# Performance work log

Hardware: AMD Instinct MI355X
Metric: run time of the kernel (lower is better)

The kernel has to match this reference:

```python
import jax, jax.numpy as jnp
import numpy as np

NUM_CORRESPONDENCES = 256
M, N, D = 8192, 8192, 256


def setup_inputs() -> dict:
    key = jax.random.key(0)
    k1, k2 = jax.random.split(key)
    ref = jax.random.normal(k1, (M, D), dtype=jnp.float32)
    src = jax.random.normal(k2, (N, D), dtype=jnp.float32)
    # pairwise_distance(normalized=True) assumes unit-norm features
    ref = ref / jnp.linalg.norm(ref, axis=-1, keepdims=True)
    src = src / jnp.linalg.norm(src, axis=-1, keepdims=True)
    return {"ref_feats": ref, "src_feats": src}


def reference(ref_feats, src_feats):
    # squared pairwise distance for normalized feats: ||r||^2 + ||s||^2 - 2 r.s = 2 - 2 r.s
    dist = 2.0 - 2.0 * jnp.einsum('md,nd->mn', ref_feats, src_feats)  # [M, N]
    scores = jnp.exp(-dist)
    # dual normalization: row-normalized * col-normalized
    ref_scores = scores / jnp.sum(scores, axis=1, keepdims=True)
    src_scores = scores / jnp.sum(scores, axis=0, keepdims=True)
    scores = ref_scores * src_scores
    n_cols = scores.shape[1]
    flat = scores.reshape(-1)
    k = min(NUM_CORRESPONDENCES, flat.shape[0])
    corr_scores, corr_indices = jax.lax.top_k(flat, k)
    ref_corr_indices = corr_indices // n_cols
    src_corr_indices = corr_indices % n_cols
    # masks are None -> ref_indices/src_indices are identity arange, no remap needed
    return ref_corr_indices, src_corr_indices, corr_scores
```

## Files before the change

### kernel.cpp

```cpp
#include <hip/hip_runtime.h>

#define MD 8192
#define ND 8192
#define DD 256
#define KTOP 256
#define CAND_T0 0.26f
#define NCAP 4096
#define NPAD 4096

typedef unsigned int u32;
typedef unsigned short u16;
typedef unsigned long long u64;

#define OFF_R    0
#define OFF_CP   65536
#define OFF_CNT  589824
#define OFF_CAND 589952
#define OFF_KEYS 606336
#define OFF_A16  655360
#define OFF_B16  (OFF_A16 + 4194304)
#define WS_REQ   (OFF_B16 + 4194304)

using f16x8 = __attribute__((ext_vector_type(8))) _Float16;
using f32x4  = __attribute__((ext_vector_type(4))) float;

#define AS1 __attribute__((address_space(1)))
#define AS3 __attribute__((address_space(3)))

__device__ __forceinline__ u16 f2h(float x) {
  union { _Float16 h; u16 u; } v;
  v.h = (_Float16)x;
  return v.u;
}

__global__ void k_init(double* __restrict__ R, double* __restrict__ CP, int* __restrict__ cnt) {
  int stride = gridDim.x * blockDim.x;
  for (int i = blockIdx.x * blockDim.x + threadIdx.x; i < MD + 8 * ND; i += stride) {
    if (i < MD) R[i] = 0.0;
    else CP[i - MD] = 0.0;
  }
  if (blockIdx.x == 0 && threadIdx.x == 0) *cnt = 0;
}

__global__ __launch_bounds__(256) void k_prep2(
    const float* __restrict__ A, const float* __restrict__ B,
    u16* __restrict__ A16p, u16* __restrict__ B16p,
    double* __restrict__ R, double* __restrict__ CP, int* __restrict__ cnt) {
  const int gid = blockIdx.x * 256 + threadIdx.x;
  if (gid < MD) R[gid] = 0.0;
  if (gid < 8 * ND) CP[gid] = 0.0;
  if (gid == 0) *cnt = 0;

  {
    float4 v = ((const float4*)A)[gid];
    ushort4 h;
    h.x = f2h(v.x); h.y = f2h(v.y); h.z = f2h(v.z); h.w = f2h(v.w);
    ((ushort4*)A16p)[gid] = h;
  }
  {
    float4 v = ((const float4*)B)[gid];
    ushort4 h;
    h.x = f2h(v.x); h.y = f2h(v.y); h.z = f2h(v.z); h.w = f2h(v.w);
    ((ushort4*)B16p)[gid] = h;
  }
}

__global__ __launch_bounds__(256, 4) void k_gemm_mfma(
    const u16* __restrict__ A16, const u16* __restrict__ B16,
    double* __restrict__ R, double* __restrict__ CP,
    int* __restrict__ cnt, u32* __restrict__ cand, int ncap) {
  __shared__ u16 sA[2][128][32];
  __shared__ u16 sB[2][128][32];
  __shared__ float sR[2][64];
  __shared__ double sC[2][64];

  const int tid = threadIdx.x;
  const int lane = tid & 63;
  const int wid = tid >> 6;
  const int wrow = wid >> 1, wcol = wid & 1;

  const int g = blockIdx.x;
  const int xcd = g & 7;
  const int l = g >> 3;
  const int rowTile = xcd * 8 + (l & 7);
  const int colTile = l >> 3;
  const int rowBase = rowTile * 128;
  const int colBase = colTile * 128;
  double* Cmy = CP + (size_t)xcd * ND;

  const int quad = lane >> 4, lo = lane & 15;
  const int sw = (lo >> 1) & 3;
  const int cswz = (lane & 3) ^ ((lane >> 3) & 3);

  const int half = wid & 1;
  u16* lb0;
  const u16* gbl;
  if (wid < 2) {
    lb0 = &sA[0][half * 64][0];
    gbl = A16 + (size_t)(rowBase + half * 64 + (lane >> 2)) * DD + cswz * 8;
  } else {
    lb0 = &sB[0][half * 64][0];
    gbl = B16 + (size_t)(colBase + half * 64 + (lane >> 2)) * DD + cswz * 8;
  }

#define STAGE(b, kt) \
  do { \
    _Pragma("unroll") \
    for (int ch = 0; ch < 4; ++ch) { \
      const u16* gp = gbl + (size_t)(ch * 16) * DD + (kt) * 32; \
      __builtin_amdgcn_global_load_lds((const AS1 void*)gp, \
          (AS3 void*)(lb0 + (b) * 4096 + ch * 512), 16, 0, 0); \
    } \
  } while (0)

  f32x4 acc[4][4];
#pragma unroll
  for (int i = 0; i < 4; ++i)
#pragma unroll
    for (int j = 0; j < 4; ++j) acc[i][j] = (f32x4){0.f, 0.f, 0.f, 0.f};

  const int cq = (quad ^ sw) * 8;

  STAGE(0, 0);
  __syncthreads();

#pragma unroll
  for (int kt = 0; kt < 8; ++kt) {
    const int cur = kt & 1;
    if (kt < 7) STAGE(cur ^ 1, kt + 1);

    f16x8 fa[4];
#pragma unroll
    for (int t = 0; t < 4; ++t)
      fa[t] = *(const f16x8*)&sA[cur][wrow * 64 + t * 16 + lo][cq];
#pragma unroll
    for (int j = 0; j < 4; ++j) {
      f16x8 fb = *(const f16x8*)&sB[cur][wcol * 64 + j * 16 + lo][cq];
#pragma unroll
      for (int i = 0; i < 4; ++i)
        acc[i][j] = __builtin_amdgcn_mfma_f32_16x16x32_f16(fa[i], fb, acc[i][j], 0, 0, 0);
    }
    __syncthreads();
  }
#undef STAGE

  float rowp[4][4];
  double colp[4];
#pragma unroll
  for (int i = 0; i < 4; ++i)
#pragma unroll
    for (int r = 0; r < 4; ++r) rowp[i][r] = 0.f;
#pragma unroll
  for (int j = 0; j < 4; ++j) colp[j] = 0.0;

#pragma unroll
  for (int i = 0; i < 4; ++i)
#pragma unroll
    for (int j = 0; j < 4; ++j)
#pragma unroll
      for (int r = 0; r < 4; ++r) {
        float c = acc[i][j][r];
        float e = __expf(2.f * c - 2.f);
        rowp[i][r] += e;
        colp[j] += (double)e;
        if (c >= CAND_T0) {
          int row = rowBase + wrow * 64 + i * 16 + quad * 4 + r;
          int col = colBase + wcol * 64 + j * 16 + lo;
          int idx = atomicAdd(cnt, 1);
          if (idx < ncap) cand[idx] = ((u32)row << 13) | (u32)col;
        }
      }

#pragma unroll
  for (int i = 0; i < 4; ++i)
#pragma unroll
    for (int r = 0; r < 4; ++r) {
      float v = rowp[i][r];
#pragma unroll
      for (int off = 8; off; off >>= 1) v += __shfl_xor(v, off, 16);
      rowp[i][r] = v;
    }
#pragma unroll
  for (int j = 0; j < 4; ++j) {
    double v = colp[j];
    v += __shfl_xor(v, 16);
    v += __shfl_xor(v, 32);
    colp[j] = v;
  }

  if (wcol == 1 && lo == 0) {
#pragma unroll
    for (int i = 0; i < 4; ++i)
#pragma unroll
      for (int r = 0; r < 4; ++r) sR[wrow][i * 16 + quad * 4 + r] = rowp[i][r];
  }
  if (wrow == 1 && quad == 0) {
#pragma unroll
    for (int j = 0; j < 4; ++j) sC[wcol][j * 16 + lo] = colp[j];
  }
  __syncthreads();

  if (wcol == 0 && lo == 0) {
#pragma unroll
    for (int i = 0; i < 4; ++i)
#pragma unroll
      for (int r = 0; r < 4; ++r) {
        int idx = i * 16 + quad * 4 + r;
        atomicAdd(&R[rowBase + wrow * 64 + idx], (double)(rowp[i][r] + sR[wrow][idx]));
      }
  }
  if (wrow == 0 && quad == 0) {
#pragma unroll
    for (int j = 0; j < 4; ++j) {
      int idx = j * 16 + lo;
      atomicAdd(&Cmy[colBase + wcol * 64 + idx], colp[j] + sC[wcol][idx]);
    }
  }
}

__global__ __launch_bounds__(256) void k_gemm_f32(
    const float* __restrict__ A, const float* __restrict__ B,
    double* __restrict__ R, double* __restrict__ CP,
    int* __restrict__ cnt, u32* __restrict__ cand, int ncap) {
  __shared__ float As[32][128];
  __shared__ float Bs[32][128];
  __shared__ double colLds[16][128];
  const int tid = threadIdx.x;
  const int tx = tid & 15, ty = tid >> 4;
  const int rowBase = blockIdx.y * 128;
  const int colBase = blockIdx.x * 128;
  float acc[8][8];
#pragma unroll
  for (int i = 0; i < 8; ++i)
#pragma unroll
    for (int j = 0; j < 8; ++j) acc[i][j] = 0.f;
  const int lr = tid >> 3;
  const int lc = (tid & 7) << 2;
  for (int kk = 0; kk < DD; kk += 32) {
#pragma unroll
    for (int r = 0; r < 4; ++r) {
      int row = lr + r * 32;
      float4 av = *(const float4*)(A + (size_t)(rowBase + row) * DD + kk + lc);
      float4 bv = *(const float4*)(B + (size_t)(colBase + row) * DD + kk + lc);
      As[lc + 0][row] = av.x; As[lc + 1][row] = av.y; As[lc + 2][row] = av.z; As[lc + 3][row] = av.w;
      Bs[lc + 0][row] = bv.x; Bs[lc + 1][row] = bv.y; Bs[lc + 2][row] = bv.z; Bs[lc + 3][row] = bv.w;
    }
    __syncthreads();
#pragma unroll 4
    for (int k = 0; k < 32; ++k) {
      float a[8], b[8];
      *(float4*)(a + 0) = *(const float4*)(&As[k][ty * 8 + 0]);
      *(float4*)(a + 4) = *(const float4*)(&As[k][ty * 8 + 4]);
      *(float4*)(b + 0) = *(const float4*)(&Bs[k][tx * 8 + 0]);
      *(float4*)(b + 4) = *(const float4*)(&Bs[k][tx * 8 + 4]);
#pragma unroll
      for (int i = 0; i < 8; ++i)
#pragma unroll
        for (int j = 0; j < 8; ++j)
          acc[i][j] = fmaf(a[i], b[j], acc[i][j]);
    }
    __syncthreads();
  }
  double colpart[8];
#pragma unroll
  for (int j = 0; j < 8; ++j) colpart[j] = 0.0;
#pragma unroll
  for (int i = 0; i < 8; ++i) {
    double rp = 0.0;
#pragma unroll
    for (int j = 0; j < 8; ++j) {
      float e = __expf(2.f * acc[i][j] - 2.f);
      rp += (double)e;
      colpart[j] += (double)e;
    }
#pragma unroll
    for (int off = 8; off; off >>= 1) rp += __shfl_down(rp, off, 16);
    if (tx == 0) atomicAdd(&R[rowBase + ty * 8 + i], rp);
  }
#pragma unroll
  for (int j = 0; j < 8; ++j) colLds[ty][tx * 8 + j] = colpart[j];
  __syncthreads();
  if (tid < 128) {
    double s = 0.0;
#pragma unroll
    for (int t = 0; t < 16; ++t) s += colLds[t][tid];
    atomicAdd(&CP[colBase + tid], s);
  }
#pragma unroll
  for (int i = 0; i < 8; ++i)
#pragma unroll
    for (int j = 0; j < 8; ++j) {
      if (acc[i][j] >= CAND_T0) {
        int idx = atomicAdd(cnt, 1);
        if (idx < ncap)
          cand[idx] = ((u32)(rowBase + ty * 8 + i) << 13) | (u32)(colBase + tx * 8 + j);
      }
    }
}

__global__ __launch_bounds__(256) void k_score(
    const float* __restrict__ A, const float* __restrict__ B,
    const double* __restrict__ R, const double* __restrict__ CP,
    const int* __restrict__ cnt, const u32* __restrict__ cand,
    u64* __restrict__ keys, int ncap) {
  int w = (int)((blockIdx.x * 256 + threadIdx.x) >> 6);
  int lane = threadIdx.x & 63;
  int n = *cnt; if (n > ncap) n = ncap;
  if (w >= n) return;
  u32 mn = cand[w];
  int m = (int)(mn >> 13), nn = (int)(mn & 8191u);
  const float* ar = A + (size_t)m * DD;
  const float* br = B + (size_t)nn * DD;
  double s = 0.0;
#pragma unroll
  for (int d = 0; d < DD; d += 64)
    s = fma((double)ar[d + lane], (double)br[d + lane], s);
#pragma unroll
  for (int off = 32; off; off >>= 1) s += __shfl_down(s, off);
  if (lane == 0) {
    double Cn = 0.0;
#pragma unroll
    for (int x = 0; x < 8; ++x) Cn += CP[(size_t)x * ND + nn];
    double sc = exp(4.0 * s - 4.0) / (R[m] * Cn);
    keys[w] = (u64)__double_as_longlong(sc);
  }
}

__device__ __forceinline__ bool is_worse(u64 ka, u32 ma, u64 kb, u32 mb) {
  return (ka < kb) || (ka == kb && ma > mb);
}

__global__ __launch_bounds__(1024) void k_sort(
    const int* __restrict__ cnt, const u32* __restrict__ cand,
    const u64* __restrict__ keys, float* __restrict__ out, int ncap) {
  __shared__ u64 sk[NPAD];
  __shared__ u32 sm[NPAD];
  const int tid = threadIdx.x;
  const int lane = tid & 63;
  const int wid = tid >> 6;
  int m = *cnt; if (m > ncap) m = ncap;

  if (m <= 2048) {
    const int NP = (m <= 1024) ? 1024 : 2048;
    const int base = wid * 128;
    const int i0 = base + lane * 2;

    u64 k0 = (i0 < m) ? keys[i0] : 0;
    u64 k1 = (i0 + 1 < m) ? keys[i0 + 1] : 0;
    u32 m0 = (i0 < m) ? cand[i0] : 0xFFFFFFFFu;
    u32 m1 = (i0 + 1 < m) ? cand[i0 + 1] : 0xFFFFFFFFu;
#pragma unroll
    for (int k = 2; k <= 128; k <<= 1) {
#pragma unroll
      for (int j = k >> 1; j >= 1; j >>= 1) {
        const bool bf = ((i0 & k) == 0);
        if (j == 1) {
          bool sw = bf ? is_worse(k0, m0, k1, m1) : is_worse(k1, m1, k0, m0);
          if (sw) { u64 tk = k0; k0 = k1; k1 = tk; u32 tm = m0; m0 = m1; m1 = tm; }
        } else {
          const int j2 = j >> 1;
          const bool keepb = (bf == ((lane & j2) == 0));
          u64 pk0 = __shfl_xor(k0, j2); u32 pm0 = __shfl_xor(m0, j2);
          u64 pk1 = __shfl_xor(k1, j2); u32 pm1 = __shfl_xor(m1, j2);
          if (keepb == is_worse(k0, m0, pk0, pm0)) { k0 = pk0; m0 = pm0; }
          if (keepb == is_worse(k1, m1, pk1, pm1)) { k1 = pk1; m1 = pm1; }
        }
      }
    }
    sk[i0] = k0; sk[i0 + 1] = k1; sm[i0] = m0; sm[i0 + 1] = m1;
    __syncthreads();

    for (int k = 256; k <= NP; k <<= 1) {
      for (int j = k >> 1; j >= 128; j >>= 1) {
        for (int i = tid; i < NP; i += 1024) {
          int l = i ^ j;
          if (l > i) {
            u64 ki = sk[i], kl = sk[l];
            u32 mi = sm[i], ml = sm[l];
            bool bf = ((i & k) == 0);
            bool swp = bf ? is_worse(ki, mi, kl, ml) : is_worse(kl, ml, ki, mi);
            if (swp) { sk[i] = kl; sk[l] = ki; sm[i] = ml; sm[l] = mi; }
          }
        }
        __syncthreads();
      }
      if (i0 < NP) {
        k0 = sk[i0]; k1 = sk[i0 + 1]; m0 = sm[i0]; m1 = sm[i0 + 1];
        const bool bf = ((base & k) == 0);
#pragma unroll
        for (int j = 64; j >= 2; j >>= 1) {
          const int j2 = j >> 1;
          const bool keepb = (bf == ((lane & j2) == 0));
          u64 pk0 = __shfl_xor(k0, j2); u32 pm0 = __shfl_xor(m0, j2);
          u64 pk1 = __shfl_xor(k1, j2); u32 pm1 = __shfl_xor(m1, j2);
          if (keepb == is_worse(k0, m0, pk0, pm0)) { k0 = pk0; m0 = pm0; }
          if (keepb == is_worse(k1, m1, pk1, pm1)) { k1 = pk1; m1 = pm1; }
        }
        {
          bool sw = bf ? is_worse(k0, m0, k1, m1) : is_worse(k1, m1, k0, m0);
          if (sw) { u64 tk = k0; k0 = k1; k1 = tk; u32 tm = m0; m0 = m1; m1 = tm; }
        }
      }
      __syncthreads();
      if (i0 < NP) { sk[i0] = k0; sk[i0 + 1] = k1; sm[i0] = m0; sm[i0 + 1] = m1; }
      __syncthreads();
    }
  } else {
    for (int i = tid; i < NPAD; i += 1024) { sk[i] = 0; sm[i] = 0xFFFFFFFFu; }
    __syncthreads();
    for (int i = tid; i < m; i += 1024) { sk[i] = keys[i]; sm[i] = cand[i]; }
    __syncthreads();
    for (unsigned k = 2; k <= (unsigned)NPAD; k <<= 1) {
      for (unsigned j = k >> 1; j > 0; j >>= 1) {
        for (unsigned i = tid; i < (unsigned)NPAD; i += 1024) {
          unsigned l = i ^ j;
          if (l > i) {
            u64 ki = sk[i], kl = sk[l];
            u32 mi = sm[i], ml = sm[l];
            bool dir = ((i & k) == 0);
            bool swp = dir ? is_worse(ki, mi, kl, ml) : is_worse(kl, ml, ki, mi);
            if (swp) { sk[i] = kl; sk[l] = ki; sm[i] = ml; sm[l] = mi; }
          }
        }
        __syncthreads();
      }
    }
  }

  for (int r = tid; r < KTOP; r += 1024) {
    u32 mn = sm[r];
    u64 kk = sk[r];
    out[r] = (float)(mn >> 13);
    out[KTOP + r] = (float)(mn & 8191u);
    out[2 * KTOP + r] = (float)__longlong_as_double((long long)kk);
  }
}

extern "C" void kernel_launch(void* const* d_in, const int* in_sizes, int n_in,
                              void* d_out, int out_size, void* d_ws, size_t ws_size,
                              hipStream_t stream) {
  (void)in_sizes; (void)n_in; (void)out_size;
  const float* A = (const float*)d_in[0];
  const float* B = (const float*)d_in[1];
  float* out = (float*)d_out;
  char* ws = (char*)d_ws;
  double* R = (double*)(ws + OFF_R);
  double* CP = (double*)(ws + OFF_CP);
  int* cnt = (int*)(ws + OFF_CNT);
  u32* cand = (u32*)(ws + OFF_CAND);
  u64* keys = (u64*)(ws + OFF_KEYS);

  if (ws_size >= (size_t)WS_REQ) {
    u16* A16p = (u16*)(ws + OFF_A16);
    u16* B16p = (u16*)(ws + OFF_B16);
    hipLaunchKernelGGL(k_prep2, dim3(2048), dim3(256), 0, stream,
                       A, B, A16p, B16p, R, CP, cnt);
    hipLaunchKernelGGL(k_gemm_mfma, dim3(4096), dim3(256), 0, stream,
                       A16p, B16p, R, CP, cnt, cand, NCAP);
  } else {
    hipLaunchKernelGGL(k_init, dim3(288), dim3(256), 0, stream, R, CP, cnt);
    hipLaunchKernelGGL(k_gemm_f32, dim3(ND / 128, MD / 128), dim3(256), 0, stream,
                       A, B, R, CP, cnt, cand, NCAP);
  }

  hipLaunchKernelGGL(k_score, dim3(NCAP / 4), dim3(256), 0, stream,
                     A, B, R, CP, cnt, cand, keys, NCAP);
  hipLaunchKernelGGL(k_sort, dim3(1), dim3(1024), 0, stream,
                     cnt, cand, keys, out, NCAP);
}
```

Measured before the change: 134.4 us.

## Process four column tiles per GEMM block and accumulate row sums in registers

Each MFMA GEMM block now sweeps four consecutive 128-column tiles instead of one, so the grid shrinks from 4096 to 1024 blocks. Row exp-sums are kept in registers across the four tiles, which cuts the double-precision row atomics by four. The first k-slice of the next tile is prefetched during the last k-step of the current one, so loads overlap across tiles. The A tile is still reloaded from global memory for every column tile, and the sweep adds a loop with an extra barrier per tile.

```diff
diff --git a/kernel.cpp b/kernel.cpp
--- a/kernel.cpp
+++ b/kernel.cpp
@@ -83,9 +83,9 @@
   const int xcd = g & 7;
   const int l = g >> 3;
   const int rowTile = xcd * 8 + (l & 7);
-  const int colTile = l >> 3;
+  const int colGroup = l >> 3;
   const int rowBase = rowTile * 128;
-  const int colBase = colTile * 128;
+  const int colBase = colGroup * 512;
   double* Cmy = CP + (size_t)xcd * ND;
 
   const int quad = lane >> 4, lo = lane & 15;
@@ -94,82 +94,109 @@
 
   const int half = wid & 1;
   u16* lb0;
-  const u16* gbl;
+  const u16* gb;
+  size_t psstride;
   if (wid < 2) {
     lb0 = &sA[0][half * 64][0];
-    gbl = A16 + (size_t)(rowBase + half * 64 + (lane >> 2)) * DD + cswz * 8;
+    gb = A16 + (size_t)(rowBase + half * 64 + (lane >> 2)) * DD + cswz * 8;
+    psstride = 0;
   } else {
     lb0 = &sB[0][half * 64][0];
-    gbl = B16 + (size_t)(colBase + half * 64 + (lane >> 2)) * DD + cswz * 8;
-  }
-
-#define STAGE(b, kt) \
+    gb = B16 + (size_t)(colBase + half * 64 + (lane >> 2)) * DD + cswz * 8;
+    psstride = (size_t)128 * DD;
+  }
+
+#define STAGE(b, kt, ps) \
   do { \
     _Pragma("unroll") \
     for (int ch = 0; ch < 4; ++ch) { \
-      const u16* gp = gbl + (size_t)(ch * 16) * DD + (kt) * 32; \
+      const u16* gp = gb + (size_t)(ps) * psstride + (size_t)(ch * 16) * DD + (kt) * 32; \
       __builtin_amdgcn_global_load_lds((const AS1 void*)gp, \
           (AS3 void*)(lb0 + (b) * 4096 + ch * 512), 16, 0, 0); \
     } \
   } while (0)
 
-  f32x4 acc[4][4];
+  const int cq = (quad ^ sw) * 8;
+
+  float rowp[4][4];
 #pragma unroll
   for (int i = 0; i < 4; ++i)
 #pragma unroll
-    for (int j = 0; j < 4; ++j) acc[i][j] = (f32x4){0.f, 0.f, 0.f, 0.f};
-
-  const int cq = (quad ^ sw) * 8;
-
-  STAGE(0, 0);
+    for (int r = 0; r < 4; ++r) rowp[i][r] = 0.f;
+
+  STAGE(0, 0, 0);
   __syncthreads();
 
-#pragma unroll
-  for (int kt = 0; kt < 8; ++kt) {
-    const int cur = kt & 1;
-    if (kt < 7) STAGE(cur ^ 1, kt + 1);
-
-    f16x8 fa[4];
-#pragma unroll
-    for (int t = 0; t < 4; ++t)
-      fa[t] = *(const f16x8*)&sA[cur][wrow * 64 + t * 16 + lo][cq];
+  for (int ps = 0; ps < 4; ++ps) {
+    f32x4 acc[4][4];
+#pragma unroll
+    for (int i = 0; i < 4; ++i)
+#pragma unroll
+      for (int j = 0; j < 4; ++j) acc[i][j] = (f32x4){0.f, 0.f, 0.f, 0.f};
+
+#pragma unroll
+    for (int kt = 0; kt < 8; ++kt) {
+      const int cur = kt & 1;
+      if (kt < 7) STAGE(cur ^ 1, kt + 1, ps);
+      else if (ps < 3) STAGE(cur ^ 1, 0, ps + 1);
+
+      f16x8 fa[4];
+#pragma unroll
+      for (int t = 0; t < 4; ++t)
+        fa[t] = *(const f16x8*)&sA[cur][wrow * 64 + t * 16 + lo][cq];
+#pragma unroll
+      for (int j = 0; j < 4; ++j) {
+        f16x8 fb = *(const f16x8*)&sB[cur][wcol * 64 + j * 16 + lo][cq];
+#pragma unroll
+        for (int i = 0; i < 4; ++i)
+          acc[i][j] = __builtin_amdgcn_mfma_f32_16x16x32_f16(fa[i], fb, acc[i][j], 0, 0, 0);
+      }
+      __syncthreads();
+    }
+
+    const int pcol = colBase + ps * 128;
+    double colp[4];
+#pragma unroll
+    for (int j = 0; j < 4; ++j) colp[j] = 0.0;
+
+#pragma unroll
+    for (int i = 0; i < 4; ++i)
+#pragma unroll
+      for (int j = 0; j < 4; ++j)
+#pragma unroll
+        for (int r = 0; r < 4; ++r) {
+          float c = acc[i][j][r];
+          float e = __expf(2.f * c - 2.f);
+          rowp[i][r] += e;
+          colp[j] += (double)e;
+          if (c >= CAND_T0) {
+            int row = rowBase + wrow * 64 + i * 16 + quad * 4 + r;
+            int col = pcol + wcol * 64 + j * 16 + lo;
+            int idx = atomicAdd(cnt, 1);
+            if (idx < ncap) cand[idx] = ((u32)row << 13) | (u32)col;
+          }
+        }
+
 #pragma unroll
     for (int j = 0; j < 4; ++j) {
-      f16x8 fb = *(const f16x8*)&sB[cur][wcol * 64 + j * 16 + lo][cq];
-#pragma unroll
-      for (int i = 0; i < 4; ++i)
-        acc[i][j] = __builtin_amdgcn_mfma_f32_16x16x32_f16(fa[i], fb, acc[i][j], 0, 0, 0);
-    }
-    __syncthreads();
-  }
-#undef STAGE
-
-  float rowp[4][4];
-  double colp[4];
-#pragma unroll
-  for (int i = 0; i < 4; ++i)
-#pragma unroll
-    for (int r = 0; r < 4; ++r) rowp[i][r] = 0.f;
-#pragma unroll
-  for (int j = 0; j < 4; ++j) colp[j] = 0.0;
-
-#pragma unroll
-  for (int i = 0; i < 4; ++i)
-#pragma unroll
-    for (int j = 0; j < 4; ++j)
-#pragma unroll
-      for (int r = 0; r < 4; ++r) {
-        float c = acc[i][j][r];
-        float e = __expf(2.f * c - 2.f);
-        rowp[i][r] += e;
-        colp[j] += (double)e;
-        if (c >= CAND_T0) {
-          int row = rowBase + wrow * 64 + i * 16 + quad * 4 + r;
-          int col = colBase + wcol * 64 + j * 16 + lo;
-          int idx = atomicAdd(cnt, 1);
-          if (idx < ncap) cand[idx] = ((u32)row << 13) | (u32)col;
-        }
-      }
+      double v = colp[j];
+      v += __shfl_xor(v, 16);
+      v += __shfl_xor(v, 32);
+      colp[j] = v;
+    }
+    if (wrow == 1 && quad == 0) {
+#pragma unroll
+      for (int j = 0; j < 4; ++j) sC[wcol][j * 16 + lo] = colp[j];
+    }
+    __syncthreads();
+    if (wrow == 0 && quad == 0) {
+#pragma unroll
+      for (int j = 0; j < 4; ++j) {
+        int idx = j * 16 + lo;
+        atomicAdd(&Cmy[pcol + wcol * 64 + idx], colp[j] + sC[wcol][idx]);
+      }
+    }
+  }
 
 #pragma unroll
   for (int i = 0; i < 4; ++i)
@@ -180,26 +207,13 @@
       for (int off = 8; off; off >>= 1) v += __shfl_xor(v, off, 16);
       rowp[i][r] = v;
     }
-#pragma unroll
-  for (int j = 0; j < 4; ++j) {
-    double v = colp[j];
-    v += __shfl_xor(v, 16);
-    v += __shfl_xor(v, 32);
-    colp[j] = v;
-  }
-
   if (wcol == 1 && lo == 0) {
 #pragma unroll
     for (int i = 0; i < 4; ++i)
 #pragma unroll
       for (int r = 0; r < 4; ++r) sR[wrow][i * 16 + quad * 4 + r] = rowp[i][r];
   }
-  if (wrow == 1 && quad == 0) {
-#pragma unroll
-    for (int j = 0; j < 4; ++j) sC[wcol][j * 16 + lo] = colp[j];
-  }
   __syncthreads();
-
   if (wcol == 0 && lo == 0) {
 #pragma unroll
     for (int i = 0; i < 4; ++i)
@@ -209,13 +223,7 @@
         atomicAdd(&R[rowBase + wrow * 64 + idx], (double)(rowp[i][r] + sR[wrow][idx]));
       }
   }
-  if (wrow == 0 && quad == 0) {
-#pragma unroll
-    for (int j = 0; j < 4; ++j) {
-      int idx = j * 16 + lo;
-      atomicAdd(&Cmy[colBase + wcol * 64 + idx], colp[j] + sC[wcol][idx]);
-    }
-  }
+#undef STAGE
 }
 
 __global__ __launch_bounds__(256) void k_gemm_f32(
@@ -455,7 +463,7 @@
     u16* B16p = (u16*)(ws + OFF_B16);
     hipLaunchKernelGGL(k_prep2, dim3(2048), dim3(256), 0, stream,
                        A, B, A16p, B16p, R, CP, cnt);
-    hipLaunchKernelGGL(k_gemm_mfma, dim3(4096), dim3(256), 0, stream,
+    hipLaunchKernelGGL(k_gemm_mfma, dim3(1024), dim3(256), 0, stream,
                        A16p, B16p, R, CP, cnt, cand, NCAP);
   } else {
     hipLaunchKernelGGL(k_init, dim3(288), dim3(256), 0, stream, R, CP, cnt);
```

Result: slower. 149.0 us (+10.8%).
